# Performance work log

Hardware: AMD Instinct MI355X
Metric: run time of the kernel (lower is better)

## Reference

```python
import jax, jax.numpy as jnp
import numpy as np

N, E, DIN, DH, DOUT, NG = 50000, 800000, 128, 128, 64, 128
EPS = 1e-5
SLOPE = 0.2  # PyG GATConv default negative_slope


def _gat(x, src, dst, W, a_s, a_d, b, heads, out_c, concat):
    n = x.shape[0]
    xp = (x @ W).reshape(n, heads, out_c)            # [N,H,C]
    e_src = (xp * a_s[None]).sum(-1)                  # [N,H]
    e_dst = (xp * a_d[None]).sum(-1)                  # [N,H]
    al = e_src[src] + e_dst[dst]                      # [E,H]
    al = jnp.where(al > 0, al, SLOPE * al)            # leaky_relu
    amax = jax.ops.segment_max(al, dst, num_segments=n)
    w = jnp.exp(al - amax[dst])                       # segment softmax (stable)
    den = jax.ops.segment_sum(w, dst, num_segments=n)
    msg = w[:, :, None] * xp[src]                     # [E,H,C]
    out = jax.ops.segment_sum(msg, dst, num_segments=n) / den[:, :, None]
    out = out.reshape(n, heads * out_c) if concat else out.mean(axis=1)
    return out + b


def _bn(h, g, be):
    m = h.mean(axis=0)
    v = h.var(axis=0)  # biased var, as in torch BN training mode
    return (h - m) / jnp.sqrt(v + EPS) * g + be


def setup_inputs() -> dict:
    key = jax.random.key(0)
    ks = jax.random.split(key, 12)
    x = jax.random.normal(ks[0], (N, DIN), dtype=jnp.float32)
    edge_index = jax.random.randint(ks[1], (2, E), 0, N, dtype=jnp.int64)
    graph_pool = jax.random.uniform(ks[2], (NG, N), dtype=jnp.float32) * (2.0 / N)
    s = 0.1
    return {
        "x": x, "edge_index": edge_index, "graph_pool": graph_pool,
        "W1": jax.random.normal(ks[3], (DIN, DH), dtype=jnp.float32) * s,
        "as1": jax.random.normal(ks[4], (1, DH), dtype=jnp.float32) * s,
        "ad1": jax.random.normal(ks[5], (1, DH), dtype=jnp.float32) * s,
        "b1": jnp.zeros((DH,), jnp.float32),
        "g1": jnp.ones((DH,), jnp.float32), "be1": jnp.zeros((DH,), jnp.float32),
        "W2": jax.random.normal(ks[6], (DH, DH), dtype=jnp.float32) * s,
        "as2": jax.random.normal(ks[7], (1, DH), dtype=jnp.float32) * s,
        "ad2": jax.random.normal(ks[8], (1, DH), dtype=jnp.float32) * s,
        "b2": jnp.zeros((DH,), jnp.float32),
        "g2": jnp.ones((DH,), jnp.float32), "be2": jnp.zeros((DH,), jnp.float32),
        "W3": jax.random.normal(ks[9], (DH, DOUT), dtype=jnp.float32) * s,
        "as3": jax.random.normal(ks[10], (1, DOUT), dtype=jnp.float32) * s,
        "ad3": jax.random.normal(ks[11], (1, DOUT), dtype=jnp.float32) * s,
        "b3": jnp.zeros((DOUT,), jnp.float32),
    }


def reference(x, edge_index, graph_pool,
              W1, as1, ad1, b1, g1, be1,
              W2, as2, ad2, b2, g2, be2,
              W3, as3, ad3, b3):
    n = x.shape[0]
    loops = jnp.arange(n, dtype=edge_index.dtype)  # PyG add_self_loops=True
    src = jnp.concatenate([edge_index[0], loops])
    dst = jnp.concatenate([edge_index[1], loops])
    h = _gat(x, src, dst, W1, as1, ad1, b1, 1, DH, True)
    h = jax.nn.relu(_bn(h, g1, be1))
    h = _gat(h, src, dst, W2, as2, ad2, b2, 1, DH, True)
    h = jax.nn.relu(_bn(h, g2, be2))
    h_nodes = _gat(h, src, dst, W3, as3, ad3, b3, 1, DOUT, False)
    h_pooled = graph_pool @ h_nodes  # sparse.mm == matmul mathematically
    return (h_pooled, h_nodes)
```

## Files before the change

kernel.cpp:

```cpp
#include <hip/hip_runtime.h>
#include <hip/hip_bf16.h>

#define DIN 128
#define DH  128
#define DOUT 64
#define NGR 128
#define EPSV 1e-5f
#define SLOPE 0.2f
#define BSH 7
#define NBMAX 512
#define BCAP 3584
#define POOLB 256
#define BNSPREAD 32

typedef __attribute__((ext_vector_type(8))) short short8;
typedef __attribute__((ext_vector_type(4))) float float4v;

__device__ __forceinline__ unsigned short f2bf(float f) {
    union { float f; unsigned int u; } v; v.f = f;
    unsigned int r = (v.u + 0x7FFFu + ((v.u >> 16) & 1u)) >> 16;
    return (unsigned short)r;
}
__device__ __forceinline__ unsigned short f2bf_f(float f) {
    return (unsigned short)((__float_as_uint(f) + 0x8000u) >> 16);
}
__device__ __forceinline__ float bf_lo(unsigned int u) { return __uint_as_float(u << 16); }
__device__ __forceinline__ float bf_hi(unsigned int u) { return __uint_as_float(u & 0xFFFF0000u); }

__device__ __forceinline__ void pack_one(const float* W, unsigned short* PW, int cout, int t) {
    int lane = t & 63;
    int ks   = (t >> 6) & 3;
    int nt   = t >> 8;
    int nn   = nt * 16 + (lane & 15);
    int k0   = ks * 32 + (lane >> 4) * 8;
    unsigned int pk[4];
#pragma unroll
    for (int p = 0; p < 4; ++p) {
        unsigned short lo = f2bf(W[(k0 + 2 * p) * cout + nn]);
        unsigned short hi = f2bf(W[(k0 + 2 * p + 1) * cout + nn]);
        pk[p] = ((unsigned int)hi << 16) | lo;
    }
    *(uint4*)&PW[(size_t)t * 8] = make_uint4(pk[0], pk[1], pk[2], pk[3]);
}

__global__ __launch_bounds__(256) void front_a_kernel(
    const int* __restrict__ ei, int* __restrict__ bucket_cnt, int2* __restrict__ binned,
    int E, int T, int nb, int binBlocks,
    const float* __restrict__ W1, unsigned short* __restrict__ PW1,
    const float* __restrict__ W2, unsigned short* __restrict__ PW2,
    const float* __restrict__ W3, unsigned short* __restrict__ PW3)
{
    if ((int)blockIdx.x >= binBlocks) {
        int t = ((int)blockIdx.x - binBlocks) * 256 + (int)threadIdx.x;
        if (t < 2048)      pack_one(W1, PW1, 128, t);
        else if (t < 4096) pack_one(W2, PW2, 128, t - 2048);
        else if (t < 5120) pack_one(W3, PW3, 64,  t - 4096);
        return;
    }
    __shared__ int hist[NBMAX], base[NBMAX], cur[NBMAX];
    for (int i = threadIdx.x; i < nb; i += 256) hist[i] = 0;
    __syncthreads();
    int start = blockIdx.x * 8192;
    int endc  = start + 8192; if (endc > T) endc = T;
    for (int e = start + threadIdx.x; e < endc; e += 256) {
        int d = (e < E) ? ei[E + e] : (e - E);
        atomicAdd(&hist[d >> BSH], 1);
    }
    __syncthreads();
    for (int i = threadIdx.x; i < nb; i += 256) {
        int h = hist[i];
        cur[i] = 0;
        if (h) base[i] = atomicAdd(&bucket_cnt[i], h);
    }
    __syncthreads();
    for (int e = start + threadIdx.x; e < endc; e += 256) {
        int s, d;
        if (e < E) { s = ei[e]; d = ei[E + e]; }
        else       { s = e - E; d = s; }
        int b = d >> BSH;
        int off = atomicAdd(&cur[b], 1);
        binned[(size_t)b * BCAP + base[b] + off] = make_int2(s, d);
    }
}

template <int COUT, int BNIN>
__device__ __forceinline__ void gemm_es_body(
    unsigned short* Xs, float* sSc, float* sSh, int row0,
    const void* __restrict__ Xv, const unsigned short* __restrict__ PW,
    const float* __restrict__ a_s, const float* __restrict__ a_d,
    const float* __restrict__ bnsum, const float* __restrict__ g,
    const float* __restrict__ be, float invn,
    unsigned short* __restrict__ XPB, float* __restrict__ e_src, float* __restrict__ e_dst, int n)
{
    constexpr int NT = COUT / 16;
    int tid = threadIdx.x;

    if constexpr (BNIN) {
        if (tid < 128) {
            float s = 0.f, q = 0.f;
#pragma unroll 4
            for (int k = 0; k < BNSPREAD; ++k) {
                s += bnsum[k * 256 + tid];
                q += bnsum[k * 256 + 128 + tid];
            }
            float mean = s * invn;
            float var  = q * invn - mean * mean;
            float sc   = g[tid] * rsqrtf(var + EPSV);
            sSc[tid] = sc;
            sSh[tid] = be[tid] - mean * sc;
        }
        __syncthreads();
        const unsigned short* H = (const unsigned short*)Xv;
        for (int i = tid; i < 64 * 16; i += 256) {
            int r  = i >> 4;
            int c8 = (i & 15) * 8;
            uint4 u = make_uint4(0, 0, 0, 0);
            if (row0 + r < n) u = *(const uint4*)&H[(size_t)(row0 + r) * 128 + c8];
            unsigned int uu[4] = {u.x, u.y, u.z, u.w};
            unsigned int out[4];
#pragma unroll
            for (int p = 0; p < 4; ++p) {
                int c = c8 + 2 * p;
                float a  = fmaxf(bf_lo(uu[p]) * sSc[c] + sSh[c], 0.f);
                float bq = fmaxf(bf_hi(uu[p]) * sSc[c + 1] + sSh[c + 1], 0.f);
                out[p] = ((unsigned int)f2bf_f(bq) << 16) | f2bf_f(a);
            }
            *(uint4*)&Xs[r * 136 + c8] = make_uint4(out[0], out[1], out[2], out[3]);
        }
    } else {
        const float* X = (const float*)Xv;
        for (int i = tid; i < 64 * 32; i += 256) {
            int r  = i >> 5;
            int k4 = (i & 31) * 4;
            float4 v = make_float4(0.f, 0.f, 0.f, 0.f);
            if (row0 + r < n) v = *(const float4*)&X[(size_t)(row0 + r) * 128 + k4];
            uint2 pk;
            pk.x = ((unsigned int)f2bf_f(v.y) << 16) | f2bf_f(v.x);
            pk.y = ((unsigned int)f2bf_f(v.w) << 16) | f2bf_f(v.z);
            *(uint2*)&Xs[r * 136 + k4] = pk;
        }
    }
    __syncthreads();

    int wv   = tid >> 6;
    int lane = tid & 63;
    int m0   = wv * 16;
    int cl   = lane & 15;
    int q    = lane >> 4;

    float4v acc[NT] = {};
#pragma unroll
    for (int ks = 0; ks < 4; ++ks) {
        short8 af = *(const short8*)&Xs[(m0 + cl) * 136 + ks * 32 + q * 8];
#pragma unroll
        for (int nt = 0; nt < NT; ++nt) {
            short8 bf = *(const short8*)&PW[(size_t)((nt * 4 + ks) * 64 + lane) * 8];
            acc[nt] = __builtin_amdgcn_mfma_f32_16x16x32_bf16(af, bf, acc[nt], 0, 0, 0);
        }
    }

    float asv[NT], adv[NT];
#pragma unroll
    for (int nt = 0; nt < NT; ++nt) {
        asv[nt] = a_s[nt * 16 + cl];
        adv[nt] = a_d[nt * 16 + cl];
    }
#pragma unroll
    for (int reg = 0; reg < 4; ++reg) {
        int m = row0 + m0 + q * 4 + reg;
        if (m >= n) continue;
        float ps = 0.f, pd = 0.f;
        size_t base = (size_t)m * COUT;
#pragma unroll
        for (int nt = 0; nt < NT; ++nt) {
            float v = acc[nt][reg];
            XPB[base + nt * 16 + cl] = f2bf_f(v);
            ps += v * asv[nt];
            pd += v * adv[nt];
        }
        ps += __shfl_xor(ps, 1); pd += __shfl_xor(pd, 1);
        ps += __shfl_xor(ps, 2); pd += __shfl_xor(pd, 2);
        ps += __shfl_xor(ps, 4); pd += __shfl_xor(pd, 4);
        ps += __shfl_xor(ps, 8); pd += __shfl_xor(pd, 8);
        if (cl == 0) {
            e_src[m] = ps;
            e_dst[m] = pd;
        }
    }
}

template <int COUT, int BNIN>
__global__ __launch_bounds__(256) void gemm_es_kernel(
    const void* __restrict__ Xv, const unsigned short* __restrict__ PW,
    const float* __restrict__ a_s, const float* __restrict__ a_d,
    const float* __restrict__ bnsum, const float* __restrict__ g,
    const float* __restrict__ be, float invn,
    unsigned short* __restrict__ XPB, float* __restrict__ e_src, float* __restrict__ e_dst, int n)
{
    __shared__ unsigned short Xs[64 * 136];
    __shared__ float sSc[128], sSh[128];
    gemm_es_body<COUT, BNIN>(Xs, sSc, sSh, blockIdx.x * 64,
                             Xv, PW, a_s, a_d, bnsum, g, be, invn, XPB, e_src, e_dst, n);
}

__global__ __launch_bounds__(256) void front_b_kernel(
    const int2* __restrict__ binned, const int* __restrict__ bucket_cnt,
    int* __restrict__ row_ptr, int* __restrict__ col_src, int n, int T, int nbcsr,
    const float* __restrict__ X, const unsigned short* __restrict__ PW,
    const float* __restrict__ a_s, const float* __restrict__ a_d,
    unsigned short* __restrict__ XPB, float* __restrict__ e_src, float* __restrict__ e_dst)
{
    __shared__ __align__(16) char smraw[64 * 136 * 2];
    int tid = threadIdx.x;

    if ((int)blockIdx.x < nbcsr) {
        int* cnt = (int*)smraw;
        int* rnk = cnt + 128;
        int* rp  = rnk + 128;
        int* sc  = rp + 128;
        int* red = sc + 128;
        int b = blockIdx.x;
        int node0 = b << BSH;
        const int2* bin = &binned[(size_t)b * BCAP];
        int nb_edges = bucket_cnt[b];

        int part = 0;
        for (int i = tid; i < b; i += 256) part += bucket_cnt[i];
        red[tid] = part;
        if (tid < 128) cnt[tid] = 0;
        __syncthreads();
#pragma unroll
        for (int s2 = 128; s2 > 0; s2 >>= 1) {
            if (tid < s2) red[tid] += red[tid + s2];
            __syncthreads();
        }
        int lo = red[0];

        for (int i = tid; i < nb_edges; i += 256)
            atomicAdd(&cnt[bin[i].y - node0], 1);
        __syncthreads();
        if (tid < 128) sc[tid] = cnt[tid];
        __syncthreads();
        for (int d2 = 1; d2 < 128; d2 <<= 1) {
            int t = 0;
            if (tid < 128 && tid >= d2) t = sc[tid - d2];
            __syncthreads();
            if (tid < 128) sc[tid] += t;
            __syncthreads();
        }
        if (tid < 128) {
            int excl = sc[tid] - cnt[tid];
            int r = lo + excl;
            rp[tid] = r;
            rnk[tid] = 0;
            int node = node0 + tid;
            if (node < n) row_ptr[node] = r;
        }
        if (b == 0 && tid == 0) row_ptr[n] = T;
        __syncthreads();
        for (int i = tid; i < nb_edges; i += 256) {
            int2 e = bin[i];
            int local = e.y - node0;
            int r = atomicAdd(&rnk[local], 1);
            col_src[rp[local] + r] = e.x;
        }
    } else {
        unsigned short* Xs = (unsigned short*)smraw;
        gemm_es_body<128, 0>(Xs, nullptr, nullptr, ((int)blockIdx.x - nbcsr) * 64,
                             X, PW, a_s, a_d, nullptr, nullptr, nullptr, 0.f,
                             XPB, e_src, e_dst, n);
    }
}

template <int COUT, int OUTBF, int BNOUT>
__global__ __launch_bounds__(256) void gat_aggregate_kernel(
    const unsigned short* __restrict__ XPB, const float* __restrict__ e_src,
    const float* __restrict__ e_dst, const int* __restrict__ row_ptr,
    const int* __restrict__ col_src, const float* __restrict__ bias,
    void* __restrict__ OUT, unsigned short* __restrict__ HNT,
    float* __restrict__ bnsumS, int n)
{
    __shared__ float bnsh[BNOUT ? 512 : 1];
    constexpr int GSH  = (COUT == 128) ? 4 : 3;
    constexpr int STEP = 64 >> GSH;
    constexpr int RSH  = (COUT == 128) ? 7 : 6;

    int wave = threadIdx.x >> 6;
    int lane = threadIdx.x & 63;
    int g    = lane >> GSH;
    int cl   = lane & ((1 << GSH) - 1);
    int d = blockIdx.x * 4 + wave;
    bool act = (d < n);
    if (!BNOUT && !act) return;

    int start = 0, end = 0;
    float ed = 0.f;
    if (act) {
        start = row_ptr[d];
        end   = row_ptr[d + 1];
        ed    = e_dst[d];
    }

    float denl = 0.f;
    float acc8[8] = {};

    for (int base = start; base < end; base += 64) {
        int t = base + lane;
        int s_l = 0; float w_l = 0.f;
        if (t < end) {
            s_l = col_src[t];
            float a = e_src[s_l] + ed;
            a = (a > 0.f) ? a : SLOPE * a;
            w_l = __expf(a);
        }
        denl += w_l;
        int cnt = end - base; if (cnt > 64) cnt = 64;

        int j = 0;
        for (; j + 16 <= cnt; j += 16) {
            int   r0 = __shfl(s_l, j + g);
            int   r1 = __shfl(s_l, j + STEP + g);
            float w0 = __shfl(w_l, j + g);
            float w1 = __shfl(w_l, j + STEP + g);
            uint4 u0 = ((const uint4*)(XPB + ((size_t)(unsigned)r0 << RSH)))[cl];
            uint4 u1 = ((const uint4*)(XPB + ((size_t)(unsigned)r1 << RSH)))[cl];
            int   r2, r3; float w2, w3; uint4 u2, u3;
            if (COUT == 128) {
                r2 = __shfl(s_l, j + 2 * STEP + g);
                r3 = __shfl(s_l, j + 3 * STEP + g);
                w2 = __shfl(w_l, j + 2 * STEP + g);
                w3 = __shfl(w_l, j + 3 * STEP + g);
                u2 = ((const uint4*)(XPB + ((size_t)(unsigned)r2 << RSH)))[cl];
                u3 = ((const uint4*)(XPB + ((size_t)(unsigned)r3 << RSH)))[cl];
            }
            unsigned int a0[4] = {u0.x, u0.y, u0.z, u0.w};
            unsigned int a1[4] = {u1.x, u1.y, u1.z, u1.w};
#pragma unroll
            for (int p = 0; p < 4; ++p) {
                acc8[2 * p]     += w0 * bf_lo(a0[p]);
                acc8[2 * p + 1] += w0 * bf_hi(a0[p]);
                acc8[2 * p]     += w1 * bf_lo(a1[p]);
                acc8[2 * p + 1] += w1 * bf_hi(a1[p]);
            }
            if (COUT == 128) {
                unsigned int a2[4] = {u2.x, u2.y, u2.z, u2.w};
                unsigned int a3[4] = {u3.x, u3.y, u3.z, u3.w};
#pragma unroll
                for (int p = 0; p < 4; ++p) {
                    acc8[2 * p]     += w2 * bf_lo(a2[p]);
                    acc8[2 * p + 1] += w2 * bf_hi(a2[p]);
                    acc8[2 * p]     += w3 * bf_lo(a3[p]);
                    acc8[2 * p + 1] += w3 * bf_hi(a3[p]);
                }
            }
        }
        for (; j < cnt; j += STEP) {
            int   r = __shfl(s_l, j + g);
            float w = __shfl(w_l, j + g);
            uint4 u = ((const uint4*)(XPB + ((size_t)(unsigned)r << RSH)))[cl];
            unsigned int au[4] = {u.x, u.y, u.z, u.w};
#pragma unroll
            for (int p = 0; p < 4; ++p) {
                acc8[2 * p]     += w * bf_lo(au[p]);
                acc8[2 * p + 1] += w * bf_hi(au[p]);
            }
        }
    }

#pragma unroll
    for (int off = (1 << GSH); off < 64; off <<= 1)
#pragma unroll
        for (int k = 0; k < 8; ++k) acc8[k] += __shfl_xor(acc8[k], off);

#pragma unroll
    for (int off = 1; off < 64; off <<= 1) denl += __shfl_xor(denl, off);
    float inv = 1.f / denl;

    float ox[8];
#pragma unroll
    for (int k = 0; k < 8; ++k) ox[k] = 0.f;
    if (act) {
#pragma unroll
        for (int k = 0; k < 8; ++k) ox[k] = acc8[k] * inv + bias[cl * 8 + k];
    }

    if (COUT == 128) {
        if (act && g == 0) {
            if (OUTBF) {
                unsigned int o0 = ((unsigned int)f2bf_f(ox[1]) << 16) | f2bf_f(ox[0]);
                unsigned int o1 = ((unsigned int)f2bf_f(ox[3]) << 16) | f2bf_f(ox[2]);
                unsigned int o2 = ((unsigned int)f2bf_f(ox[5]) << 16) | f2bf_f(ox[4]);
                unsigned int o3 = ((unsigned int)f2bf_f(ox[7]) << 16) | f2bf_f(ox[6]);
                ((uint4*)OUT)[(size_t)d * 16 + cl] = make_uint4(o0, o1, o2, o3);
            } else {
                ((float4*)OUT)[(size_t)d * 32 + cl * 2]     = make_float4(ox[0], ox[1], ox[2], ox[3]);
                ((float4*)OUT)[(size_t)d * 32 + cl * 2 + 1] = make_float4(ox[4], ox[5], ox[6], ox[7]);
            }
        }
        if (BNOUT) {
            if (g == 0) {
#pragma unroll
                for (int k = 0; k < 8; ++k) bnsh[wave * 128 + cl * 8 + k] = ox[k];
            }
            __syncthreads();
            if (wave == 0) {
                float s0 = 0.f, q0 = 0.f, s1 = 0.f, q1 = 0.f;
#pragma unroll
                for (int k = 0; k < 4; ++k) {
                    float v0 = bnsh[k * 128 + 2 * lane];
                    float v1 = bnsh[k * 128 + 2 * lane + 1];
                    s0 += v0; q0 += v0 * v0;
                    s1 += v1; q1 += v1 * v1;
                }
                float* dstb = &bnsumS[(blockIdx.x & (BNSPREAD - 1)) * 256];
                atomicAdd(&dstb[2 * lane],           s0);
                atomicAdd(&dstb[2 * lane + 1],       s1);
                atomicAdd(&dstb[128 + 2 * lane],     q0);
                atomicAdd(&dstb[128 + 2 * lane + 1], q1);
            }
        }
    } else {
        if (act && g == 0) {
            ((float4*)OUT)[(size_t)d * 16 + cl * 2]     = make_float4(ox[0], ox[1], ox[2], ox[3]);
            ((float4*)OUT)[(size_t)d * 16 + cl * 2 + 1] = make_float4(ox[4], ox[5], ox[6], ox[7]);
#pragma unroll
            for (int k = 0; k < 8; ++k)
                HNT[(size_t)(cl * 8 + k) * n + d] = f2bf_f(ox[k]);
        }
    }
}

__global__ __launch_bounds__(256) void pool_mfma_kernel(
    const float* __restrict__ GP, const unsigned short* __restrict__ HNT,
    float* __restrict__ partial, int n, int nchunk)
{
    __shared__ unsigned short gp_s[128 * 136];
    __shared__ unsigned short ht_s[64 * 136];
    int tid = threadIdx.x;
    int wv = tid >> 6, lane = tid & 63, cl = lane & 15, q = lane >> 4;

    float4v acc[4][2] = {};

    for (int blk = blockIdx.x; blk < nchunk; blk += gridDim.x) {
        int k0 = blk * 128;

        for (int i = tid; i < 128 * 8; i += 256) {
            int r  = i >> 3;
            int kk = (i & 7) * 16;
            int gk = k0 + kk;
            const float* src = &GP[(size_t)r * n + gk];
            unsigned int pk[8];
#pragma unroll
            for (int q2 = 0; q2 < 4; ++q2) {
                float4 v = make_float4(0.f, 0.f, 0.f, 0.f);
                if (gk + q2 * 4 < n) v = *(const float4*)&src[q2 * 4];
                pk[2 * q2 + 0] = ((unsigned int)f2bf_f(v.y) << 16) | f2bf_f(v.x);
                pk[2 * q2 + 1] = ((unsigned int)f2bf_f(v.w) << 16) | f2bf_f(v.z);
            }
            *(uint4*)&gp_s[r * 136 + kk]     = make_uint4(pk[0], pk[1], pk[2], pk[3]);
            *(uint4*)&gp_s[r * 136 + kk + 8] = make_uint4(pk[4], pk[5], pk[6], pk[7]);
        }
        for (int i = tid; i < 64 * 16; i += 256) {
            int r  = i >> 4;
            int kk = (i & 15) * 8;
            int gk = k0 + kk;
            uint4 v = make_uint4(0, 0, 0, 0);
            if (gk < n) v = *(const uint4*)&HNT[(size_t)r * n + gk];
            *(uint4*)&ht_s[r * 136 + kk] = v;
        }
        __syncthreads();

#pragma unroll
        for (int ks = 0; ks < 4; ++ks) {
            short8 bfr[2];
#pragma unroll
            for (int j = 0; j < 2; ++j)
                bfr[j] = *(const short8*)&gp_s[((wv * 2 + j) * 16 + cl) * 136 + ks * 32 + q * 8];
#pragma unroll
            for (int mt = 0; mt < 4; ++mt) {
                short8 af = *(const short8*)&ht_s[(mt * 16 + cl) * 136 + ks * 32 + q * 8];
#pragma unroll
                for (int j = 0; j < 2; ++j)
                    acc[mt][j] = __builtin_amdgcn_mfma_f32_16x16x32_bf16(af, bfr[j], acc[mt][j], 0, 0, 0);
            }
        }
        __syncthreads();
    }

    float* po = &partial[(size_t)blockIdx.x * (NGR * DOUT)];
#pragma unroll
    for (int mt = 0; mt < 4; ++mt) {
#pragma unroll
        for (int j = 0; j < 2; ++j) {
            int g = (wv * 2 + j) * 16 + cl;
            int c = mt * 16 + q * 4;
            *(float4*)&po[g * 64 + c] =
                make_float4(acc[mt][j][0], acc[mt][j][1], acc[mt][j][2], acc[mt][j][3]);
        }
    }
}

__global__ __launch_bounds__(256) void pool_reduce_kernel(
    const float* __restrict__ partial, float* __restrict__ OUT, int nblk)
{
    int i = blockIdx.x * 256 + threadIdx.x;
    float s0 = 0.f, s1 = 0.f, s2 = 0.f, s3 = 0.f;
    int p = 0;
    for (; p + 3 < nblk; p += 4) {
        s0 += partial[(size_t)(p + 0) * (NGR * DOUT) + i];
        s1 += partial[(size_t)(p + 1) * (NGR * DOUT) + i];
        s2 += partial[(size_t)(p + 2) * (NGR * DOUT) + i];
        s3 += partial[(size_t)(p + 3) * (NGR * DOUT) + i];
    }
    for (; p < nblk; ++p) s0 += partial[(size_t)p * (NGR * DOUT) + i];
    OUT[i] = (s0 + s1) + (s2 + s3);
}

extern "C" void kernel_launch(void* const* d_in, const int* in_sizes, int n_in,
                              void* d_out, int out_size, void* d_ws, size_t ws_size,
                              hipStream_t stream) {
    const float* x   = (const float*)d_in[0];
    const int*   ei  = (const int*)d_in[1];
    const float* gp  = (const float*)d_in[2];
    const float* W1  = (const float*)d_in[3];
    const float* as1 = (const float*)d_in[4];
    const float* ad1 = (const float*)d_in[5];
    const float* b1  = (const float*)d_in[6];
    const float* g1  = (const float*)d_in[7];
    const float* be1 = (const float*)d_in[8];
    const float* W2  = (const float*)d_in[9];
    const float* as2 = (const float*)d_in[10];
    const float* ad2 = (const float*)d_in[11];
    const float* b2  = (const float*)d_in[12];
    const float* g2  = (const float*)d_in[13];
    const float* be2 = (const float*)d_in[14];
    const float* W3  = (const float*)d_in[15];
    const float* as3 = (const float*)d_in[16];
    const float* ad3 = (const float*)d_in[17];
    const float* b3  = (const float*)d_in[18];

    const int N = in_sizes[0] / DIN;
    const int E = in_sizes[1] / 2;
    const int T = E + N;
    const int NB = (N + 127) >> BSH;

    char* ws = (char*)d_ws;
    auto take = [&](size_t bytes) {
        char* p = ws;
        ws += (bytes + 511) & ~(size_t)511;
        return p;
    };
    unsigned short* xpb = (unsigned short*)take((size_t)N * 128 * 2);
    unsigned short* h   = (unsigned short*)take((size_t)N * 128 * 2);
    unsigned short* hnt = (unsigned short*)take((size_t)64 * N * 2);
    float* pool_s  = (float*)take((size_t)POOLB * NGR * DOUT * 4);
    float* esd     = (float*)take((size_t)2 * N * 4);
    float* e_src   = esd;
    float* e_dst   = esd + N;
    int*   row_ptr = (int*)take((size_t)(N + 1) * 4);
    int*   col_src = (int*)take((size_t)T * 4);
    int2*  binned  = (int2*)take((size_t)NB * BCAP * 8);
    int*   zero_rgn   = (int*)take((size_t)(NBMAX + 1 + 2 * BNSPREAD * 256) * 4);
    int*   bucket_cnt = zero_rgn;
    float* bnsum1     = (float*)(zero_rgn + NBMAX + 1);
    float* bnsum2     = bnsum1 + BNSPREAD * 256;
    unsigned short* pw1 = (unsigned short*)take((size_t)128 * 128 * 2);
    unsigned short* pw2 = (unsigned short*)take((size_t)128 * 128 * 2);
    unsigned short* pw3 = (unsigned short*)take((size_t)128 * 64 * 2);

    float* outp = (float*)d_out;
    float* hn   = outp + NGR * DOUT;

    hipMemsetAsync(zero_rgn, 0, (size_t)(NBMAX + 1 + 2 * BNSPREAD * 256) * 4, stream);

    const int binBlocks = (T + 8191) / 8192;
    front_a_kernel<<<binBlocks + 20, 256, 0, stream>>>(ei, bucket_cnt, binned, E, T, NB, binBlocks,
                                                       W1, pw1, W2, pw2, W3, pw3);

    const int gx = (N + 63) / 64;
    const float invn = 1.f / N;

    front_b_kernel<<<NB + gx, 256, 0, stream>>>(binned, bucket_cnt, row_ptr, col_src, N, T, NB,
                                                x, pw1, as1, ad1, xpb, e_src, e_dst);

    gat_aggregate_kernel<128, 1, 1><<<(N + 3) / 4, 256, 0, stream>>>(
        xpb, e_src, e_dst, row_ptr, col_src, b1, h, nullptr, bnsum1, N);

    gemm_es_kernel<128, 1><<<gx, 256, 0, stream>>>(h, pw2, as2, ad2,
        bnsum1, g1, be1, invn, xpb, e_src, e_dst, N);
    gat_aggregate_kernel<128, 1, 1><<<(N + 3) / 4, 256, 0, stream>>>(
        xpb, e_src, e_dst, row_ptr, col_src, b2, h, nullptr, bnsum2, N);

    gemm_es_kernel<64, 1><<<gx, 256, 0, stream>>>(h, pw3, as3, ad3,
        bnsum2, g2, be2, invn, xpb, e_src, e_dst, N);
    gat_aggregate_kernel<64, 0, 0><<<(N + 3) / 4, 256, 0, stream>>>(
        xpb, e_src, e_dst, row_ptr, col_src, b3, hn, hnt, nullptr, N);

    const int nchunk = (N + 127) / 128;
    const int pb = nchunk < POOLB ? nchunk : POOLB;
    pool_mfma_kernel<<<pb, 256, 0, stream>>>(gp, hnt, pool_s, N, nchunk);
    pool_reduce_kernel<<<(NGR * DOUT + 255) / 256, 256, 0, stream>>>(pool_s, outp, pb);
}
```

Baseline: 344.1 us.

## Pre-convert graph_pool to bf16 in front kernel and drop transposed HNT store

The fp32→bf16 conversion of the 128×N graph_pool matrix moves out of the pool kernel into extra blocks of the first kernel, where it can overlap with edge binning. The pool kernel then reads bf16 GP directly and transposes h_nodes from the fp32 output in shared memory. This removes the strided transposed HNT writes from the last aggregate. The binning chunk size is also halved to give more blocks. The cost is an extra bf16 write and re-read of graph_pool, about 12.8 MB, plus scattered shared-memory transposes.

```diff
diff --git a/kernel.cpp b/kernel.cpp
--- a/kernel.cpp
+++ b/kernel.cpp
@@ -12,6 +12,7 @@
 #define BCAP 3584
 #define POOLB 256
 #define BNSPREAD 32
+#define BINCH 4096
 
 typedef __attribute__((ext_vector_type(8))) short short8;
 typedef __attribute__((ext_vector_type(4))) float float4v;
@@ -48,10 +49,36 @@
     int E, int T, int nb, int binBlocks,
     const float* __restrict__ W1, unsigned short* __restrict__ PW1,
     const float* __restrict__ W2, unsigned short* __restrict__ PW2,
-    const float* __restrict__ W3, unsigned short* __restrict__ PW3)
+    const float* __restrict__ W3, unsigned short* __restrict__ PW3,
+    const float* __restrict__ GP, unsigned short* __restrict__ GPB, int n)
 {
-    if ((int)blockIdx.x >= binBlocks) {
-        int t = ((int)blockIdx.x - binBlocks) * 256 + (int)threadIdx.x;
+    int blk = (int)blockIdx.x;
+    if (blk >= binBlocks + 20) {
+        size_t t = (size_t)(blk - binBlocks - 20) * 256 + threadIdx.x;
+        size_t base = t * 32;
+        size_t tot = (size_t)NGR * (size_t)n;
+        if (base >= tot) return;
+        if (base + 32 <= tot) {
+            const float* src = GP + base;
+            unsigned short* dst = GPB + base;
+#pragma unroll
+            for (int q2 = 0; q2 < 4; ++q2) {
+                float4 a = *(const float4*)&src[q2 * 8];
+                float4 b = *(const float4*)&src[q2 * 8 + 4];
+                uint4 o;
+                o.x = ((unsigned int)f2bf_f(a.y) << 16) | f2bf_f(a.x);
+                o.y = ((unsigned int)f2bf_f(a.w) << 16) | f2bf_f(a.z);
+                o.z = ((unsigned int)f2bf_f(b.y) << 16) | f2bf_f(b.x);
+                o.w = ((unsigned int)f2bf_f(b.w) << 16) | f2bf_f(b.z);
+                *(uint4*)&dst[q2 * 8] = o;
+            }
+        } else {
+            for (size_t k = base; k < tot; ++k) GPB[k] = f2bf_f(GP[k]);
+        }
+        return;
+    }
+    if (blk >= binBlocks) {
+        int t = (blk - binBlocks) * 256 + (int)threadIdx.x;
         if (t < 2048)      pack_one(W1, PW1, 128, t);
         else if (t < 4096) pack_one(W2, PW2, 128, t - 2048);
         else if (t < 5120) pack_one(W3, PW3, 64,  t - 4096);
@@ -60,8 +87,8 @@
     __shared__ int hist[NBMAX], base[NBMAX], cur[NBMAX];
     for (int i = threadIdx.x; i < nb; i += 256) hist[i] = 0;
     __syncthreads();
-    int start = blockIdx.x * 8192;
-    int endc  = start + 8192; if (endc > T) endc = T;
+    int start = blk * BINCH;
+    int endc  = start + BINCH; if (endc > T) endc = T;
     for (int e = start + threadIdx.x; e < endc; e += 256) {
         int d = (e < E) ? ei[E + e] : (e - E);
         atomicAdd(&hist[d >> BSH], 1);
@@ -277,8 +304,7 @@
     const unsigned short* __restrict__ XPB, const float* __restrict__ e_src,
     const float* __restrict__ e_dst, const int* __restrict__ row_ptr,
     const int* __restrict__ col_src, const float* __restrict__ bias,
-    void* __restrict__ OUT, unsigned short* __restrict__ HNT,
-    float* __restrict__ bnsumS, int n)
+    void* __restrict__ OUT, float* __restrict__ bnsumS, int n)
 {
     __shared__ float bnsh[BNOUT ? 512 : 1];
     constexpr int GSH  = (COUT == 128) ? 4 : 3;
@@ -423,15 +449,12 @@
         if (act && g == 0) {
             ((float4*)OUT)[(size_t)d * 16 + cl * 2]     = make_float4(ox[0], ox[1], ox[2], ox[3]);
             ((float4*)OUT)[(size_t)d * 16 + cl * 2 + 1] = make_float4(ox[4], ox[5], ox[6], ox[7]);
-#pragma unroll
-            for (int k = 0; k < 8; ++k)
-                HNT[(size_t)(cl * 8 + k) * n + d] = f2bf_f(ox[k]);
         }
     }
 }
 
 __global__ __launch_bounds__(256) void pool_mfma_kernel(
-    const float* __restrict__ GP, const unsigned short* __restrict__ HNT,
+    const unsigned short* __restrict__ GPB, const float* __restrict__ HN,
     float* __restrict__ partial, int n, int nchunk)
 {
     __shared__ unsigned short gp_s[128 * 136];
@@ -444,29 +467,32 @@
     for (int blk = blockIdx.x; blk < nchunk; blk += gridDim.x) {
         int k0 = blk * 128;
 
-        for (int i = tid; i < 128 * 8; i += 256) {
-            int r  = i >> 3;
-            int kk = (i & 7) * 16;
-            int gk = k0 + kk;
-            const float* src = &GP[(size_t)r * n + gk];
-            unsigned int pk[8];
-#pragma unroll
-            for (int q2 = 0; q2 < 4; ++q2) {
-                float4 v = make_float4(0.f, 0.f, 0.f, 0.f);
-                if (gk + q2 * 4 < n) v = *(const float4*)&src[q2 * 4];
-                pk[2 * q2 + 0] = ((unsigned int)f2bf_f(v.y) << 16) | f2bf_f(v.x);
-                pk[2 * q2 + 1] = ((unsigned int)f2bf_f(v.w) << 16) | f2bf_f(v.z);
-            }
-            *(uint4*)&gp_s[r * 136 + kk]     = make_uint4(pk[0], pk[1], pk[2], pk[3]);
-            *(uint4*)&gp_s[r * 136 + kk + 8] = make_uint4(pk[4], pk[5], pk[6], pk[7]);
-        }
-        for (int i = tid; i < 64 * 16; i += 256) {
+        for (int i = tid; i < 128 * 16; i += 256) {
             int r  = i >> 4;
             int kk = (i & 15) * 8;
             int gk = k0 + kk;
             uint4 v = make_uint4(0, 0, 0, 0);
-            if (gk < n) v = *(const uint4*)&HNT[(size_t)r * n + gk];
-            *(uint4*)&ht_s[r * 136 + kk] = v;
+            if (gk + 7 < n) {
+                v = *(const uint4*)&GPB[(size_t)r * n + gk];
+            } else if (gk < n) {
+                unsigned short tmp[8];
+#pragma unroll
+                for (int e2 = 0; e2 < 8; ++e2)
+                    tmp[e2] = (gk + e2 < n) ? GPB[(size_t)r * n + gk + e2] : 0;
+                v = *(const uint4*)tmp;
+            }
+            *(uint4*)&gp_s[r * 136 + kk] = v;
+        }
+        for (int i = tid; i < 128 * 16; i += 256) {
+            int k  = i >> 4;
+            int c4 = (i & 15) * 4;
+            int gk = k0 + k;
+            float4 v = make_float4(0.f, 0.f, 0.f, 0.f);
+            if (gk < n) v = *(const float4*)&HN[(size_t)gk * 64 + c4];
+            ht_s[(c4 + 0) * 136 + k] = f2bf_f(v.x);
+            ht_s[(c4 + 1) * 136 + k] = f2bf_f(v.y);
+            ht_s[(c4 + 2) * 136 + k] = f2bf_f(v.z);
+            ht_s[(c4 + 3) * 136 + k] = f2bf_f(v.w);
         }
         __syncthreads();
 
@@ -552,7 +578,7 @@
     };
     unsigned short* xpb = (unsigned short*)take((size_t)N * 128 * 2);
     unsigned short* h   = (unsigned short*)take((size_t)N * 128 * 2);
-    unsigned short* hnt = (unsigned short*)take((size_t)64 * N * 2);
+    unsigned short* gpb = (unsigned short*)take((size_t)NGR * N * 2);
     float* pool_s  = (float*)take((size_t)POOLB * NGR * DOUT * 4);
     float* esd     = (float*)take((size_t)2 * N * 4);
     float* e_src   = esd;
@@ -573,9 +599,11 @@
 
     hipMemsetAsync(zero_rgn, 0, (size_t)(NBMAX + 1 + 2 * BNSPREAD * 256) * 4, stream);
 
-    const int binBlocks = (T + 8191) / 8192;
-    front_a_kernel<<<binBlocks + 20, 256, 0, stream>>>(ei, bucket_cnt, binned, E, T, NB, binBlocks,
-                                                       W1, pw1, W2, pw2, W3, pw3);
+    const int binBlocks = (T + BINCH - 1) / BINCH;
+    const int gpBlocks  = (int)(((size_t)NGR * N / 32 + 255) / 256);
+    front_a_kernel<<<binBlocks + 20 + gpBlocks, 256, 0, stream>>>(
+        ei, bucket_cnt, binned, E, T, NB, binBlocks,
+        W1, pw1, W2, pw2, W3, pw3, gp, gpb, N);
 
     const int gx = (N + 63) / 64;
     const float invn = 1.f / N;
@@ -584,20 +612,20 @@
                                                 x, pw1, as1, ad1, xpb, e_src, e_dst);
 
     gat_aggregate_kernel<128, 1, 1><<<(N + 3) / 4, 256, 0, stream>>>(
-        xpb, e_src, e_dst, row_ptr, col_src, b1, h, nullptr, bnsum1, N);
+        xpb, e_src, e_dst, row_ptr, col_src, b1, h, bnsum1, N);
 
     gemm_es_kernel<128, 1><<<gx, 256, 0, stream>>>(h, pw2, as2, ad2,
         bnsum1, g1, be1, invn, xpb, e_src, e_dst, N);
     gat_aggregate_kernel<128, 1, 1><<<(N + 3) / 4, 256, 0, stream>>>(
-        xpb, e_src, e_dst, row_ptr, col_src, b2, h, nullptr, bnsum2, N);
+        xpb, e_src, e_dst, row_ptr, col_src, b2, h, bnsum2, N);
 
     gemm_es_kernel<64, 1><<<gx, 256, 0, stream>>>(h, pw3, as3, ad3,
         bnsum2, g2, be2, invn, xpb, e_src, e_dst, N);
     gat_aggregate_kernel<64, 0, 0><<<(N + 3) / 4, 256, 0, stream>>>(
-        xpb, e_src, e_dst, row_ptr, col_src, b3, hn, hnt, nullptr, N);
+        xpb, e_src, e_dst, row_ptr, col_src, b3, hn, nullptr, N);
 
     const int nchunk = (N + 127) / 128;
     const int pb = nchunk < POOLB ? nchunk : POOLB;
-    pool_mfma_kernel<<<pb, 256, 0, stream>>>(gp, hnt, pool_s, N, nchunk);
+    pool_mfma_kernel<<<pb, 256, 0, stream>>>(gpb, hn, pool_s, N, nchunk);
     pool_reduce_kernel<<<(NGR * DOUT + 255) / 256, 256, 0, stream>>>(pool_s, outp, pb);
 }
```

Measured after the change: 330.2 us. 1.04x faster.
